# Optimization experiments

Hardware: AMD Instinct MI355X
Metric: run time of the kernel (lower is better)

## Reference

```python
import jax, jax.numpy as jnp
import numpy as np

N = 100000      # nodes (single ntype)
F_IN = 128
F_OUT = 128
R = 3           # relations
E = 262144      # edges per relation
LRELU_SLOPE = 0.2


def setup_inputs() -> dict:
    key = jax.random.key(0)
    ks = jax.random.split(key, 6)
    x = jax.random.normal(ks[0], (N, F_IN), jnp.float32)
    src = jax.random.randint(ks[1], (R, E), 0, N)
    dst = jax.random.randint(ks[2], (R, E), 0, N)
    # attention: Linear(2*in_feat, 1) per relation
    att_w = jax.random.normal(ks[3], (R, 2 * F_IN, 1), jnp.float32) * 0.05
    att_b = jnp.zeros((R, 1), jnp.float32)
    # transform: Linear(in_feat, out_feat) per relation
    tw = jax.random.normal(ks[4], (R, F_IN, F_OUT), jnp.float32) * (1.0 / np.sqrt(F_IN))
    tb = jnp.zeros((R, F_OUT), jnp.float32)
    h_bias = jnp.zeros((F_OUT,), jnp.float32)
    return dict(x=x, att_w=att_w, att_b=att_b, tw=tw, tb=tb,
                h_bias=h_bias, src=src, dst=dst)


def reference(x, att_w, att_b, tw, tb, h_bias, src, dst):
    # Per-relation gather of endpoint features.  [R, E, F_IN]
    h_src = x[src]
    h_dst = x[dst]
    # attention Linear on cat([h_src, h_dst]) == split matmul (avoids concat)
    w_s, w_d = att_w[:, :F_IN, :], att_w[:, F_IN:, :]
    scores = (jnp.einsum('ref,rfo->reo', h_src, w_s)
              + jnp.einsum('ref,rfo->reo', h_dst, w_d)
              + att_b[:, None, :])                      # [R, E, 1]
    scores = jax.nn.leaky_relu(scores, negative_slope=LRELU_SLOPE)
    # Faithful to source: F.softmax(scores, dim=0) -> softmax over ALL edges
    # of a relation (NOT per-destination edge softmax).
    a = jax.nn.softmax(scores, axis=1)                  # [R, E, 1]
    # u_mul_e with node-level transform(h_src): message = (h_src @ tw + tb) * a
    msg = (jnp.einsum('ref,rfo->reo', h_src, tw) + tb[:, None, :]) * a  # [R,E,F_OUT]
    # scatter-sum to destinations per relation, then sum over relations
    agg = jax.vmap(lambda m, d: jax.ops.segment_sum(m, d, num_segments=N))(msg, dst)
    h = agg.sum(axis=0) + h_bias                        # [N, F_OUT]
    # activation=relu, dropout=0.0 (identity)
    return jax.nn.relu(h)
```

## Files before the change

### kernel.cpp

```cpp
#include <hip/hip_runtime.h>
#include <hip/hip_bf16.h>

#define N_NODES 100000
#define FDIM 128
#define RREL 3
#define NEDGE 262144
#define SLOPE 0.2f
#define NCHUNK 98
#define PROJ_BLOCKS 782
#define HIST_BLOCKS (RREL * NEDGE / 256)

typedef __attribute__((ext_vector_type(8))) short bf16x8;
typedef __attribute__((ext_vector_type(8))) unsigned short u16x8;
typedef __attribute__((ext_vector_type(4))) float f32x4;
typedef __attribute__((ext_vector_type(16))) float f32x16;
typedef __attribute__((ext_vector_type(4))) int i32x4;

__device__ inline unsigned short f2bf(float f) {
    __hip_bfloat16 h = __float2bfloat16(f);
    return *reinterpret_cast<unsigned short*>(&h);
}
__device__ inline float bf2f(unsigned short u) {
    unsigned int b = ((unsigned int)u) << 16;
    return __int_as_float(b);
}

#define WS_PS    0
#define WS_PD    300000
#define WS_SUMS  600000
#define WS_COUNT 600016
#define WS_ROWS  900016
#define WS_BSUM  1200016
#define WS_ESORT 1200528
#define WS_ASUM  2773392
#define WS_TWT   3073392
#define WS_TBS   3097968
#define WS_XBF   3098352
#define WS_AGGB  9498352
#define WS_RANK  28698352

__global__ __launch_bounds__(256, 4)
void proj_hist_kernel(const float* __restrict__ x,
                      const float* __restrict__ att_w,
                      float* __restrict__ ps, float* __restrict__ pd,
                      unsigned short* __restrict__ x_bf,
                      const int* __restrict__ dst, int* __restrict__ count,
                      int* __restrict__ rank) {
    if (blockIdx.x >= PROJ_BLOCKS) {
        const int b = blockIdx.x - PROJ_BLOCKS;
        const int gid = b * 256 + threadIdx.x;
        const int r = b >> 10;
        rank[gid] = atomicAdd(&count[r * N_NODES + dst[gid]], 1);
        return;
    }
    __shared__ unsigned short sX[128 * 136];
    __shared__ unsigned short sW[16 * 136];
    const int tid = threadIdx.x;
    const int row0 = blockIdx.x * 128;

#pragma unroll
    for (int i = 0; i < 8; ++i) {
        const int idx = tid + i * 256;
        const int c = idx >> 7, k = idx & 127;
        float v = 0.f;
        if (c < 3) v = att_w[c * 256 + k];
        else if (c < 6) v = att_w[(c - 3) * 256 + 128 + k];
        sW[c * 136 + k] = f2bf(v);
    }
    const int g = tid >> 5, lane = tid & 31;
#pragma unroll
    for (int it = 0; it < 16; ++it) {
        const int rrow = it * 8 + g;
        const int row = row0 + rrow;
        float4 xv = make_float4(0.f, 0.f, 0.f, 0.f);
        if (row < N_NODES) xv = *reinterpret_cast<const float4*>(x + (size_t)row * FDIM + lane * 4);
        ushort4 u;
        u.x = f2bf(xv.x); u.y = f2bf(xv.y); u.z = f2bf(xv.z); u.w = f2bf(xv.w);
        if (row < N_NODES)
            *reinterpret_cast<ushort4*>(x_bf + (size_t)row * FDIM + lane * 4) = u;
        *reinterpret_cast<ushort4*>(&sX[rrow * 136 + lane * 4]) = u;
    }
    __syncthreads();

    const int w = tid >> 6, l = tid & 63;
    const int lr = l & 15, lk = l >> 4;
    f32x4 acc[2];
    acc[0] = (f32x4){0.f, 0.f, 0.f, 0.f};
    acc[1] = (f32x4){0.f, 0.f, 0.f, 0.f};
#pragma unroll
    for (int ks = 0; ks < 4; ++ks) {
        const bf16x8 bfr = *reinterpret_cast<const bf16x8*>(&sW[lr * 136 + ks * 32 + lk * 8]);
#pragma unroll
        for (int rt = 0; rt < 2; ++rt) {
            const bf16x8 afr =
                *reinterpret_cast<const bf16x8*>(&sX[(w * 32 + rt * 16 + lr) * 136 + ks * 32 + lk * 8]);
            acc[rt] = __builtin_amdgcn_mfma_f32_16x16x32_bf16(afr, bfr, acc[rt], 0, 0, 0);
        }
    }
    if (lr < 6) {
        float* base = (lr < 3) ? (ps + lr * N_NODES) : (pd + (lr - 3) * N_NODES);
#pragma unroll
        for (int rt = 0; rt < 2; ++rt) {
            const int rowbase = row0 + w * 32 + rt * 16 + lk * 4;
#pragma unroll
            for (int j = 0; j < 4; ++j) {
                const int row = rowbase + j;
                if (row < N_NODES) base[row] = acc[rt][j];
            }
        }
    }
}

__global__ void scan1_kernel(const int* __restrict__ count, int* __restrict__ row_start,
                             int* __restrict__ bsum) {
    const int r = blockIdx.x / NCHUNK;
    const int b = blockIdx.x % NCHUNK;
    const int tid = threadIdx.x;
    const int base = b * 1024 + tid * 4;
    int v[4];
#pragma unroll
    for (int i = 0; i < 4; ++i)
        v[i] = (base + i < N_NODES) ? count[r * N_NODES + base + i] : 0;
    const int tsum = v[0] + v[1] + v[2] + v[3];
    __shared__ int sd[256];
    sd[tid] = tsum;
    __syncthreads();
    for (int off = 1; off < 256; off <<= 1) {
        const int tv = (tid >= off) ? sd[tid - off] : 0;
        __syncthreads();
        sd[tid] += tv;
        __syncthreads();
    }
    int run = sd[tid] - tsum;
#pragma unroll
    for (int i = 0; i < 4; ++i) {
        if (base + i < N_NODES) row_start[r * N_NODES + base + i] = run;
        run += v[i];
    }
    if (tid == 255) bsum[blockIdx.x] = sd[255];
}

__global__ void scan2_kernel(int* __restrict__ bsum) {
    const int r = blockIdx.x;
    const int tid = threadIdx.x;
    const int v = (tid < NCHUNK) ? bsum[r * NCHUNK + tid] : 0;
    __shared__ int sd[256];
    sd[tid] = v;
    __syncthreads();
    for (int off = 1; off < 256; off <<= 1) {
        const int tv = (tid >= off) ? sd[tid - off] : 0;
        __syncthreads();
        sd[tid] += tv;
        __syncthreads();
    }
    if (tid < NCHUNK) bsum[r * NCHUNK + tid] = sd[tid] - v;
}

__global__ void scan3_kernel(int* __restrict__ row_start, const int* __restrict__ bsum) {
    const int r = blockIdx.x / NCHUNK;
    const int b = blockIdx.x % NCHUNK;
    const int add = bsum[blockIdx.x];
    const int base = b * 1024 + threadIdx.x * 4;
#pragma unroll
    for (int i = 0; i < 4; ++i)
        if (base + i < N_NODES) row_start[r * N_NODES + base + i] += add;
}

__global__ void fill_kernel(const int* __restrict__ src, const int* __restrict__ dst,
                            const float* __restrict__ ps, const float* __restrict__ pd,
                            const float* __restrict__ att_b,
                            const int* __restrict__ row_start, const int* __restrict__ rank,
                            int2* __restrict__ edge_sorted, float* __restrict__ sums) {
    const int gid = blockIdx.x * 256 + threadIdx.x;
    const int r = blockIdx.x >> 10;
    const int s = src[gid];
    const int d = dst[gid];
    float sc = ps[r * N_NODES + s] + pd[r * N_NODES + d] + att_b[r];
    sc = sc > 0.f ? sc : SLOPE * sc;
    const float ev = __expf(sc);
    const int pos = row_start[r * N_NODES + d] + rank[gid];
    int2 pk;
    pk.x = s;
    pk.y = __float_as_int(ev);
    edge_sorted[(size_t)r * NEDGE + pos] = pk;
    float v = ev;
#pragma unroll
    for (int off = 32; off >= 1; off >>= 1) v += __shfl_xor(v, off);
    __shared__ float red[4];
    if ((threadIdx.x & 63) == 0) red[threadIdx.x >> 6] = v;
    __syncthreads();
    if (threadIdx.x == 0) {
        unsafeAtomicAdd(&sums[r], red[0] + red[1] + red[2] + red[3]);
    }
}

__global__ void cast_kernel(const float* __restrict__ tw, const float* __restrict__ tb,
                            const float* __restrict__ sums,
                            unsigned short* __restrict__ twT, float* __restrict__ tbs) {
    const int o = blockIdx.x * 256 + threadIdx.x;
    const int elem = o & 7;
    const int lane = (o >> 3) & 63;
    const int ct   = (o >> 9) & 3;
    const int kk   = (o >> 11) & 1;
    const int ks   = o >> 12;
    const int col = ct * 32 + (lane & 31);
    const int k   = ks * 32 + kk * 16 + ((lane >> 5) << 3) + elem;
    const float inv = 1.0f / sums[k >> 7];
    twT[o] = f2bf(tw[k * 128 + col] * inv);
    if (o < 384) tbs[o] = tb[o] * (1.0f / sums[o >> 7]);
}

__global__ void agg_kernel(const int* __restrict__ row_start,
                           const int2* __restrict__ edge_sorted,
                           const unsigned short* __restrict__ x_bf,
                           unsigned short* __restrict__ aggb, float* __restrict__ asum) {
    const int lane = threadIdx.x & 15;
    const int r = blockIdx.y;
    const int n = blockIdx.x * 16 + (threadIdx.x >> 4);
    const int beg = row_start[r * N_NODES + n];
    const int end = (n == N_NODES - 1) ? NEDGE : row_start[r * N_NODES + n + 1];
    const long long* es = (const long long*)(edge_sorted + (size_t)r * NEDGE);

    float acc[8] = {0.f, 0.f, 0.f, 0.f, 0.f, 0.f, 0.f, 0.f};
    float asacc = 0.f;

    for (int i = beg; i < end; i += 4) {
        const int rem = end - i;
        long long q0, q1, q2, q3;
        q0 = __builtin_nontemporal_load(es + i);
        if (rem > 1) q1 = __builtin_nontemporal_load(es + i + 1);
        if (rem > 2) q2 = __builtin_nontemporal_load(es + i + 2);
        if (rem > 3) q3 = __builtin_nontemporal_load(es + i + 3);
        u16x8 xv0, xv1, xv2, xv3;
        xv0 = *reinterpret_cast<const u16x8*>(x_bf + (size_t)(int)q0 * FDIM + lane * 8);
        if (rem > 1) xv1 = *reinterpret_cast<const u16x8*>(x_bf + (size_t)(int)q1 * FDIM + lane * 8);
        if (rem > 2) xv2 = *reinterpret_cast<const u16x8*>(x_bf + (size_t)(int)q2 * FDIM + lane * 8);
        if (rem > 3) xv3 = *reinterpret_cast<const u16x8*>(x_bf + (size_t)(int)q3 * FDIM + lane * 8);
        {
            const float a = __int_as_float((int)(q0 >> 32));
            asacc += a;
#pragma unroll
            for (int d = 0; d < 8; ++d) acc[d] += a * bf2f(xv0[d]);
        }
        if (rem > 1) {
            const float a = __int_as_float((int)(q1 >> 32));
            asacc += a;
#pragma unroll
            for (int d = 0; d < 8; ++d) acc[d] += a * bf2f(xv1[d]);
        }
        if (rem > 2) {
            const float a = __int_as_float((int)(q2 >> 32));
            asacc += a;
#pragma unroll
            for (int d = 0; d < 8; ++d) acc[d] += a * bf2f(xv2[d]);
        }
        if (rem > 3) {
            const float a = __int_as_float((int)(q3 >> 32));
            asacc += a;
#pragma unroll
            for (int d = 0; d < 8; ++d) acc[d] += a * bf2f(xv3[d]);
        }
    }

    u16x8 o;
#pragma unroll
    for (int d = 0; d < 8; ++d) o[d] = f2bf(acc[d]);
    i32x4* dst4 = reinterpret_cast<i32x4*>(aggb + (size_t)n * 384 + r * FDIM + lane * 8);
    __builtin_nontemporal_store(*reinterpret_cast<i32x4*>(&o), dst4);
    if (lane == 0) asum[r * N_NODES + n] = asacc;
}

__global__ __launch_bounds__(1024, 4)
void gemm_kernel(const unsigned short* __restrict__ A, const unsigned short* __restrict__ Bf,
                 const float* __restrict__ asum, const float* __restrict__ tbs,
                 const float* __restrict__ h_bias, float* __restrict__ out) {
    __shared__ int4 sB[6144];
    const int tid = threadIdx.x;
    const int4* Bfv = reinterpret_cast<const int4*>(Bf);
#pragma unroll
    for (int i = 0; i < 6; ++i) sB[i * 1024 + tid] = Bfv[i * 1024 + tid];
    __syncthreads();

    const int w = tid >> 6, l = tid & 63;
    const int row = l & 31, hi = l >> 5;
    const int n0 = blockIdx.x * 512 + w * 32;
    const int arow = min(n0 + row, N_NODES - 1);
    const unsigned short* aptr = A + (size_t)arow * 384 + hi * 8;
    const unsigned short* sb = reinterpret_cast<const unsigned short*>(sB);

    f32x16 acc[4];
#pragma unroll
    for (int ct = 0; ct < 4; ++ct)
#pragma unroll
        for (int j = 0; j < 16; ++j) acc[ct][j] = 0.f;

#pragma unroll
    for (int ks = 0; ks < 12; ++ks) {
        const bf16x8 af0 = *reinterpret_cast<const bf16x8*>(aptr + ks * 32);
        const bf16x8 af1 = *reinterpret_cast<const bf16x8*>(aptr + ks * 32 + 16);
        const unsigned short* sbk = sb + ks * 4096;
#pragma unroll
        for (int ct = 0; ct < 4; ++ct) {
            const bf16x8 b0 = *reinterpret_cast<const bf16x8*>(sbk + ct * 512 + l * 8);
            acc[ct] = __builtin_amdgcn_mfma_f32_32x32x16_bf16(af0, b0, acc[ct], 0, 0, 0);
        }
#pragma unroll
        for (int ct = 0; ct < 4; ++ct) {
            const bf16x8 b1 = *reinterpret_cast<const bf16x8*>(sbk + 2048 + ct * 512 + l * 8);
            acc[ct] = __builtin_amdgcn_mfma_f32_32x32x16_bf16(af1, b1, acc[ct], 0, 0, 0);
        }
    }

    const int col = row;
    const float hb = h_bias[col];
    const float t0 = tbs[col], t1 = tbs[FDIM + col], t2 = tbs[2 * FDIM + col];
#pragma unroll
    for (int g = 0; g < 4; ++g) {
        const int rbase = n0 + g * 8 + hi * 4;
        float as0[4], as1[4], as2[4];
#pragma unroll
        for (int j = 0; j < 4; ++j) {
            const bool ok = (rbase + j) < N_NODES;
            as0[j] = ok ? asum[0 * N_NODES + rbase + j] : 0.f;
            as1[j] = ok ? asum[1 * N_NODES + rbase + j] : 0.f;
            as2[j] = ok ? asum[2 * N_NODES + rbase + j] : 0.f;
        }
#pragma unroll
        for (int ct = 0; ct < 4; ++ct) {
#pragma unroll
            for (int j = 0; j < 4; ++j) {
                const int r_ = rbase + j;
                if (r_ < N_NODES) {
                    float v = acc[ct][g * 4 + j] + as0[j] * t0 + as1[j] * t1 + as2[j] * t2 + hb;
                    out[(size_t)r_ * FDIM + ct * 32 + col] = fmaxf(v, 0.f);
                }
            }
        }
    }
}

extern "C" void kernel_launch(void* const* d_in, const int* in_sizes, int n_in,
                              void* d_out, int out_size, void* d_ws, size_t ws_size,
                              hipStream_t stream) {
    const float* x      = (const float*)d_in[0];
    const float* att_w  = (const float*)d_in[1];
    const float* att_b  = (const float*)d_in[2];
    const float* tw     = (const float*)d_in[3];
    const float* tb     = (const float*)d_in[4];
    const float* h_bias = (const float*)d_in[5];
    const int*   src    = (const int*)d_in[6];
    const int*   dst    = (const int*)d_in[7];
    float* out = (float*)d_out;

    float* wsf = (float*)d_ws;
    float* ps         = wsf + WS_PS;
    float* pd         = wsf + WS_PD;
    float* sums       = wsf + WS_SUMS;
    int*   count      = (int*)(wsf + WS_COUNT);
    int*   row_start  = (int*)(wsf + WS_ROWS);
    int*   bsum       = (int*)(wsf + WS_BSUM);
    int2*  edge_sorted= (int2*)(wsf + WS_ESORT);
    float* asum       = wsf + WS_ASUM;
    unsigned short* twT  = (unsigned short*)(wsf + WS_TWT);
    float* tbs        = wsf + WS_TBS;
    unsigned short* x_bf = (unsigned short*)(wsf + WS_XBF);
    unsigned short* aggb = (unsigned short*)(wsf + WS_AGGB);
    int*   rank       = (int*)(wsf + WS_RANK);

    hipMemsetAsync(sums, 0, 16 * sizeof(float), stream);
    hipMemsetAsync(count, 0, (size_t)RREL * N_NODES * sizeof(int), stream);

    proj_hist_kernel<<<PROJ_BLOCKS + HIST_BLOCKS, 256, 0, stream>>>(x, att_w, ps, pd, x_bf,
                                                                    dst, count, rank);

    scan1_kernel<<<RREL * NCHUNK, 256, 0, stream>>>(count, row_start, bsum);
    scan2_kernel<<<RREL, 256, 0, stream>>>(bsum);
    scan3_kernel<<<RREL * NCHUNK, 256, 0, stream>>>(row_start, bsum);

    fill_kernel<<<RREL * NEDGE / 256, 256, 0, stream>>>(src, dst, ps, pd, att_b,
                                                        row_start, rank, edge_sorted, sums);

    cast_kernel<<<192, 256, 0, stream>>>(tw, tb, sums, twT, tbs);

    agg_kernel<<<dim3(N_NODES / 16, RREL), 256, 0, stream>>>(row_start, edge_sorted, x_bf,
                                                             aggb, asum);

    gemm_kernel<<<196, 1024, 0, stream>>>(aggb, twT, asum, tbs, h_bias, out);
}
```

Baseline: 192.7 us.

## Fuse edge aggregation and per-relation GEMM into one kernel via shared memory

Merges the aggregation kernel and the transform GEMM into a single kernel. Each 512-thread block gathers and aggregates 64 nodes across all three relations into shared memory, then runs MFMA on that tile against the transposed weights held in shared memory. This drops the global round-trip of the bf16 aggregate buffer and the attention-sum array, plus one launch. In exchange each block needs about 150 KB of LDS and reloads the full 96 KB weight matrix, which limits occupancy. The gather phase also loses the overlap that many small independent blocks gave it.

Result: slower. 219.1 us (+13.7%).

```diff
diff --git a/kernel.cpp b/kernel.cpp
--- a/kernel.cpp
+++ b/kernel.cpp
@@ -36,7 +36,6 @@
 #define WS_TWT   3073392
 #define WS_TBS   3097968
 #define WS_XBF   3098352
-#define WS_AGGB  9498352
 #define WS_RANK  28698352
 
 __global__ __launch_bounds__(256, 4)
@@ -210,130 +209,116 @@
     if (o < 384) tbs[o] = tb[o] * (1.0f / sums[o >> 7]);
 }
 
-__global__ void agg_kernel(const int* __restrict__ row_start,
-                           const int2* __restrict__ edge_sorted,
-                           const unsigned short* __restrict__ x_bf,
-                           unsigned short* __restrict__ aggb, float* __restrict__ asum) {
-    const int lane = threadIdx.x & 15;
-    const int r = blockIdx.y;
-    const int n = blockIdx.x * 16 + (threadIdx.x >> 4);
-    const int beg = row_start[r * N_NODES + n];
-    const int end = (n == N_NODES - 1) ? NEDGE : row_start[r * N_NODES + n + 1];
-    const long long* es = (const long long*)(edge_sorted + (size_t)r * NEDGE);
-
-    float acc[8] = {0.f, 0.f, 0.f, 0.f, 0.f, 0.f, 0.f, 0.f};
-    float asacc = 0.f;
-
-    for (int i = beg; i < end; i += 4) {
-        const int rem = end - i;
-        long long q0, q1, q2, q3;
-        q0 = __builtin_nontemporal_load(es + i);
-        if (rem > 1) q1 = __builtin_nontemporal_load(es + i + 1);
-        if (rem > 2) q2 = __builtin_nontemporal_load(es + i + 2);
-        if (rem > 3) q3 = __builtin_nontemporal_load(es + i + 3);
-        u16x8 xv0, xv1, xv2, xv3;
-        xv0 = *reinterpret_cast<const u16x8*>(x_bf + (size_t)(int)q0 * FDIM + lane * 8);
-        if (rem > 1) xv1 = *reinterpret_cast<const u16x8*>(x_bf + (size_t)(int)q1 * FDIM + lane * 8);
-        if (rem > 2) xv2 = *reinterpret_cast<const u16x8*>(x_bf + (size_t)(int)q2 * FDIM + lane * 8);
-        if (rem > 3) xv3 = *reinterpret_cast<const u16x8*>(x_bf + (size_t)(int)q3 * FDIM + lane * 8);
-        {
-            const float a = __int_as_float((int)(q0 >> 32));
-            asacc += a;
-#pragma unroll
-            for (int d = 0; d < 8; ++d) acc[d] += a * bf2f(xv0[d]);
+__global__ __launch_bounds__(512, 2)
+void agg_gemm_kernel(const int* __restrict__ row_start,
+                     const int2* __restrict__ edge_sorted,
+                     const unsigned short* __restrict__ x_bf,
+                     const unsigned short* __restrict__ Bf,
+                     const float* __restrict__ tbs, const float* __restrict__ h_bias,
+                     float* __restrict__ out) {
+    __shared__ unsigned short sAgg[64 * 392];
+    __shared__ int4 sB[6144];
+    __shared__ float sAs[RREL][64];
+    const int tid = threadIdx.x;
+    const int n0 = blockIdx.x * 64;
+
+    const int4* Bfv = reinterpret_cast<const int4*>(Bf);
+#pragma unroll
+    for (int i = 0; i < 12; ++i) sB[i * 512 + tid] = Bfv[i * 512 + tid];
+
+    const int lane = tid & 15;
+    const int grp  = tid >> 4;
+#pragma unroll
+    for (int it = 0; it < 6; ++it) {
+        const int pair = it * 32 + grp;
+        const int r = pair >> 6;
+        const int nl = pair & 63;
+        const int n = n0 + nl;
+        if (n >= N_NODES) continue;
+        const int beg = row_start[r * N_NODES + n];
+        const int end = (n == N_NODES - 1) ? NEDGE : row_start[r * N_NODES + n + 1];
+        const long long* es = (const long long*)(edge_sorted + (size_t)r * NEDGE);
+
+        float acc[8] = {0.f, 0.f, 0.f, 0.f, 0.f, 0.f, 0.f, 0.f};
+        float asacc = 0.f;
+        for (int i = beg; i < end; i += 4) {
+            const int rem = end - i;
+            long long q0, q1, q2, q3;
+            q0 = __builtin_nontemporal_load(es + i);
+            if (rem > 1) q1 = __builtin_nontemporal_load(es + i + 1);
+            if (rem > 2) q2 = __builtin_nontemporal_load(es + i + 2);
+            if (rem > 3) q3 = __builtin_nontemporal_load(es + i + 3);
+            u16x8 xv0, xv1, xv2, xv3;
+            xv0 = *reinterpret_cast<const u16x8*>(x_bf + (size_t)(int)q0 * FDIM + lane * 8);
+            if (rem > 1) xv1 = *reinterpret_cast<const u16x8*>(x_bf + (size_t)(int)q1 * FDIM + lane * 8);
+            if (rem > 2) xv2 = *reinterpret_cast<const u16x8*>(x_bf + (size_t)(int)q2 * FDIM + lane * 8);
+            if (rem > 3) xv3 = *reinterpret_cast<const u16x8*>(x_bf + (size_t)(int)q3 * FDIM + lane * 8);
+            {
+                const float a = __int_as_float((int)(q0 >> 32));
+                asacc += a;
+#pragma unroll
+                for (int d = 0; d < 8; ++d) acc[d] += a * bf2f(xv0[d]);
+            }
+            if (rem > 1) {
+                const float a = __int_as_float((int)(q1 >> 32));
+                asacc += a;
+#pragma unroll
+                for (int d = 0; d < 8; ++d) acc[d] += a * bf2f(xv1[d]);
+            }
+            if (rem > 2) {
+                const float a = __int_as_float((int)(q2 >> 32));
+                asacc += a;
+#pragma unroll
+                for (int d = 0; d < 8; ++d) acc[d] += a * bf2f(xv2[d]);
+            }
+            if (rem > 3) {
+                const float a = __int_as_float((int)(q3 >> 32));
+                asacc += a;
+#pragma unroll
+                for (int d = 0; d < 8; ++d) acc[d] += a * bf2f(xv3[d]);
+            }
         }
-        if (rem > 1) {
-            const float a = __int_as_float((int)(q1 >> 32));
-            asacc += a;
-#pragma unroll
-            for (int d = 0; d < 8; ++d) acc[d] += a * bf2f(xv1[d]);
-        }
-        if (rem > 2) {
-            const float a = __int_as_float((int)(q2 >> 32));
-            asacc += a;
-#pragma unroll
-            for (int d = 0; d < 8; ++d) acc[d] += a * bf2f(xv2[d]);
-        }
-        if (rem > 3) {
-            const float a = __int_as_float((int)(q3 >> 32));
-            asacc += a;
-#pragma unroll
-            for (int d = 0; d < 8; ++d) acc[d] += a * bf2f(xv3[d]);
-        }
-    }
-
-    u16x8 o;
-#pragma unroll
-    for (int d = 0; d < 8; ++d) o[d] = f2bf(acc[d]);
-    i32x4* dst4 = reinterpret_cast<i32x4*>(aggb + (size_t)n * 384 + r * FDIM + lane * 8);
-    __builtin_nontemporal_store(*reinterpret_cast<i32x4*>(&o), dst4);
-    if (lane == 0) asum[r * N_NODES + n] = asacc;
-}
-
-__global__ __launch_bounds__(1024, 4)
-void gemm_kernel(const unsigned short* __restrict__ A, const unsigned short* __restrict__ Bf,
-                 const float* __restrict__ asum, const float* __restrict__ tbs,
-                 const float* __restrict__ h_bias, float* __restrict__ out) {
-    __shared__ int4 sB[6144];
-    const int tid = threadIdx.x;
-    const int4* Bfv = reinterpret_cast<const int4*>(Bf);
-#pragma unroll
-    for (int i = 0; i < 6; ++i) sB[i * 1024 + tid] = Bfv[i * 1024 + tid];
+        u16x8 o;
+#pragma unroll
+        for (int d = 0; d < 8; ++d) o[d] = f2bf(acc[d]);
+        *reinterpret_cast<u16x8*>(&sAgg[nl * 392 + r * FDIM + lane * 8]) = o;
+        if (lane == 0) sAs[r][nl] = asacc;
+    }
     __syncthreads();
 
     const int w = tid >> 6, l = tid & 63;
-    const int row = l & 31, hi = l >> 5;
-    const int n0 = blockIdx.x * 512 + w * 32;
-    const int arow = min(n0 + row, N_NODES - 1);
-    const unsigned short* aptr = A + (size_t)arow * 384 + hi * 8;
+    const int col31 = l & 31, hi = l >> 5;
+    const int rt = w & 1, ctile = w >> 1;
     const unsigned short* sb = reinterpret_cast<const unsigned short*>(sB);
 
-    f32x16 acc[4];
-#pragma unroll
-    for (int ct = 0; ct < 4; ++ct)
-#pragma unroll
-        for (int j = 0; j < 16; ++j) acc[ct][j] = 0.f;
+    f32x16 acc;
+#pragma unroll
+    for (int j = 0; j < 16; ++j) acc[j] = 0.f;
 
 #pragma unroll
     for (int ks = 0; ks < 12; ++ks) {
-        const bf16x8 af0 = *reinterpret_cast<const bf16x8*>(aptr + ks * 32);
-        const bf16x8 af1 = *reinterpret_cast<const bf16x8*>(aptr + ks * 32 + 16);
-        const unsigned short* sbk = sb + ks * 4096;
-#pragma unroll
-        for (int ct = 0; ct < 4; ++ct) {
-            const bf16x8 b0 = *reinterpret_cast<const bf16x8*>(sbk + ct * 512 + l * 8);
-            acc[ct] = __builtin_amdgcn_mfma_f32_32x32x16_bf16(af0, b0, acc[ct], 0, 0, 0);
-        }
-#pragma unroll
-        for (int ct = 0; ct < 4; ++ct) {
-            const bf16x8 b1 = *reinterpret_cast<const bf16x8*>(sbk + 2048 + ct * 512 + l * 8);
-            acc[ct] = __builtin_amdgcn_mfma_f32_32x32x16_bf16(af1, b1, acc[ct], 0, 0, 0);
-        }
-    }
-
-    const int col = row;
+        const unsigned short* arow = &sAgg[(rt * 32 + col31) * 392 + ks * 32 + hi * 8];
+        const bf16x8 af0 = *reinterpret_cast<const bf16x8*>(arow);
+        const bf16x8 af1 = *reinterpret_cast<const bf16x8*>(arow + 16);
+        const bf16x8 b0 = *reinterpret_cast<const bf16x8*>(sb + ks * 4096 + ctile * 512 + l * 8);
+        const bf16x8 b1 = *reinterpret_cast<const bf16x8*>(sb + ks * 4096 + 2048 + ctile * 512 + l * 8);
+        acc = __builtin_amdgcn_mfma_f32_32x32x16_bf16(af0, b0, acc, 0, 0, 0);
+        acc = __builtin_amdgcn_mfma_f32_32x32x16_bf16(af1, b1, acc, 0, 0, 0);
+    }
+
+    const int col = ctile * 32 + col31;
     const float hb = h_bias[col];
     const float t0 = tbs[col], t1 = tbs[FDIM + col], t2 = tbs[2 * FDIM + col];
 #pragma unroll
     for (int g = 0; g < 4; ++g) {
-        const int rbase = n0 + g * 8 + hi * 4;
-        float as0[4], as1[4], as2[4];
+        const int rlbase = rt * 32 + g * 8 + hi * 4;
 #pragma unroll
         for (int j = 0; j < 4; ++j) {
-            const bool ok = (rbase + j) < N_NODES;
-            as0[j] = ok ? asum[0 * N_NODES + rbase + j] : 0.f;
-            as1[j] = ok ? asum[1 * N_NODES + rbase + j] : 0.f;
-            as2[j] = ok ? asum[2 * N_NODES + rbase + j] : 0.f;
-        }
-#pragma unroll
-        for (int ct = 0; ct < 4; ++ct) {
-#pragma unroll
-            for (int j = 0; j < 4; ++j) {
-                const int r_ = rbase + j;
-                if (r_ < N_NODES) {
-                    float v = acc[ct][g * 4 + j] + as0[j] * t0 + as1[j] * t1 + as2[j] * t2 + hb;
-                    out[(size_t)r_ * FDIM + ct * 32 + col] = fmaxf(v, 0.f);
-                }
+            const int rl = rlbase + j;
+            const int r_ = n0 + rl;
+            if (r_ < N_NODES) {
+                float v = acc[g * 4 + j] + sAs[0][rl] * t0 + sAs[1][rl] * t1 + sAs[2][rl] * t2 + hb;
+                out[(size_t)r_ * FDIM + col] = fmaxf(v, 0.f);
             }
         }
     }
@@ -360,11 +345,9 @@
     int*   row_start  = (int*)(wsf + WS_ROWS);
     int*   bsum       = (int*)(wsf + WS_BSUM);
     int2*  edge_sorted= (int2*)(wsf + WS_ESORT);
-    float* asum       = wsf + WS_ASUM;
     unsigned short* twT  = (unsigned short*)(wsf + WS_TWT);
     float* tbs        = wsf + WS_TBS;
     unsigned short* x_bf = (unsigned short*)(wsf + WS_XBF);
-    unsigned short* aggb = (unsigned short*)(wsf + WS_AGGB);
     int*   rank       = (int*)(wsf + WS_RANK);
 
     hipMemsetAsync(sums, 0, 16 * sizeof(float), stream);
@@ -382,8 +365,6 @@
 
     cast_kernel<<<192, 256, 0, stream>>>(tw, tb, sums, twT, tbs);
 
-    agg_kernel<<<dim3(N_NODES / 16, RREL), 256, 0, stream>>>(row_start, edge_sorted, x_bf,
-                                                             aggb, asum);
-
-    gemm_kernel<<<196, 1024, 0, stream>>>(aggb, twT, asum, tbs, h_bias, out);
-}
+    agg_gemm_kernel<<<(N_NODES + 63) / 64, 512, 0, stream>>>(row_start, edge_sorted, x_bf,
+                                                             twT, tbs, h_bias, out);
+}
```
